# Optimization experiments

Measured on AMD Instinct MI355X. Metric: run time of the kernel, lower is better.

## Reference

```python
import jax, jax.numpy as jnp
import numpy as np
from jax import lax

DIM = 192
HEADS = 6
WS = 8
SHIFT = 4
RED = max(8, DIM // 8)  # 24
HID = 4 * DIM


def _rel_index(ws):
    coords = np.stack(np.meshgrid(np.arange(ws), np.arange(ws), indexing='ij'))  # [2,ws,ws]
    flat = coords.reshape(2, -1)
    rel = (flat[:, :, None] - flat[:, None, :]).transpose(1, 2, 0)  # [T,T,2]
    rel[:, :, 0] += ws - 1
    rel[:, :, 1] += ws - 1
    rel[:, :, 0] *= 2 * ws - 1
    return rel.sum(-1)  # [T,T]


def _build_mask(h, w, ws, shift):
    img = np.zeros((h, w))
    slices = (slice(0, -ws), slice(-ws, -shift), slice(-shift, None))
    cnt = 0
    for hs in slices:
        for wcs in slices:
            img[hs, wcs] = cnt
            cnt += 1
    mw = img.reshape(h // ws, ws, w // ws, ws).transpose(0, 2, 1, 3).reshape(-1, ws * ws)
    diff = mw[:, None, :] - mw[:, :, None]  # [nW,T,T], diff[w,i,j]=mw[w,j]-mw[w,i]
    return np.where(diff != 0, -100.0, 0.0).astype(np.float32)


def _ln(x, g, b):
    m = x.mean(-1, keepdims=True)
    v = ((x - m) ** 2).mean(-1, keepdims=True)
    return (x - m) / jnp.sqrt(v + 1e-5) * g + b


def _conv(x, k, b, pad):
    y = lax.conv_general_dilated(x, k, (1, 1), [(pad, pad), (pad, pad)],
                                 dimension_numbers=('NCHW', 'OIHW', 'NCHW'))
    return y + b[None, :, None, None]


def setup_inputs() -> dict:
    key = jax.random.key(0)
    ks = jax.random.split(key, 16)
    rn = lambda k, s, sc=0.02: jax.random.normal(k, s, dtype=jnp.float32) * sc
    C = DIM
    return {
        'x': jax.random.normal(ks[0], (4, 256 * 256, C), dtype=jnp.float32),
        'ln1_g': jnp.ones((C,), jnp.float32), 'ln1_b': jnp.zeros((C,), jnp.float32),
        'w_qkv': rn(ks[1], (3 * C, C)), 'b_qkv': jnp.zeros((3 * C,), jnp.float32),
        'rel_table': rn(ks[2], ((2 * WS - 1) ** 2, HEADS)),
        'w_proj': rn(ks[3], (C, C)), 'b_proj': jnp.zeros((C,), jnp.float32),
        'ln2_g': jnp.ones((C,), jnp.float32), 'ln2_b': jnp.zeros((C,), jnp.float32),
        'w_fc1': rn(ks[4], (HID, C)), 'b_fc1': jnp.zeros((HID,), jnp.float32),
        'w_fc2': rn(ks[5], (C, HID)), 'b_fc2': jnp.zeros((C,), jnp.float32),
        'conv1_w': rn(ks[6], (RED, C, 1, 1)), 'conv1_b': jnp.zeros((RED,), jnp.float32),
        'conv2_w': rn(ks[7], (RED, RED, 3, 3)), 'conv2_b': jnp.zeros((RED,), jnp.float32),
        'conv3_w': rn(ks[8], (C, RED, 1, 1)), 'conv3_b': jnp.zeros((C,), jnp.float32),
        'se_w1': rn(ks[9], (RED, C)), 'se_w2': rn(ks[10], (C, RED)),
        'h': 256, 'w': 256,
    }


def reference(x, ln1_g, ln1_b, w_qkv, b_qkv, rel_table, w_proj, b_proj,
              ln2_g, ln2_b, w_fc1, b_fc1, w_fc2, b_fc2,
              conv1_w, conv1_b, conv2_w, conv2_b, conv3_w, conv3_b,
              se_w1, se_w2, h, w):
    B, _, C = x.shape
    ws, T, nh = WS, WS * WS, HEADS
    hd = C // nh
    scale = hd ** -0.5

    nx = _ln(x, ln1_g, ln1_b).reshape(B, h, w, C)
    local = nx.transpose(0, 3, 1, 2)  # NCHW for LCE

    # shifted window attention
    sh = jnp.roll(nx, (-SHIFT, -SHIFT), axis=(1, 2))
    win = sh.reshape(B, h // ws, ws, w // ws, ws, C).transpose(0, 1, 3, 2, 4, 5).reshape(-1, T, C)
    qkv = (win @ w_qkv.T + b_qkv).reshape(-1, T, 3, nh, hd).transpose(2, 0, 3, 1, 4)
    q, k, v = qkv[0] * scale, qkv[1], qkv[2]  # [BW, nh, T, hd]
    attn = jnp.einsum('whid,whjd->whij', q, k)  # [BW, nh, T, T]
    bias = rel_table[_rel_index(ws).reshape(-1)].reshape(T, T, nh).transpose(2, 0, 1)
    attn = attn + bias[None]
    mask = jnp.asarray(_build_mask(h, w, ws, SHIFT))  # [nW, T, T]
    nW = mask.shape[0]
    attn = attn.reshape(B, nW, nh, T, T) + mask[None, :, None]
    attn = jax.nn.softmax(attn, axis=-1).reshape(-1, nh, T, T)
    out = jnp.einsum('whij,whjd->whid', attn, v).transpose(0, 2, 1, 3).reshape(-1, T, C)
    out = out @ w_proj.T + b_proj
    out = out.reshape(B, h // ws, w // ws, ws, ws, C).transpose(0, 1, 3, 2, 4, 5).reshape(B, h, w, C)
    out = jnp.roll(out, (SHIFT, SHIFT), axis=(1, 2))

    x1 = x + out.reshape(B, h * w, C)
    n2 = _ln(x1, ln2_g, ln2_b)
    mlp = jax.nn.gelu(n2 @ w_fc1.T + b_fc1, approximate=False) @ w_fc2.T + b_fc2
    x2 = x1 + mlp

    # LocalContextExtractor (SE-style)
    y = _conv(local, conv1_w, conv1_b, 0)
    y = _conv(y, conv2_w, conv2_b, 1)
    y = _conv(y, conv3_w, conv3_b, 0)
    y = jnp.where(y >= 0, y, 0.2 * y)  # LeakyReLU(0.2)
    pooled = y.mean(axis=(2, 3))  # [B, C]
    wgt = jax.nn.sigmoid(jax.nn.relu(pooled @ se_w1.T) @ se_w2.T)
    y = y * wgt[:, :, None, None]
    lc = y.reshape(B, C, h * w).transpose(0, 2, 1)
    return x2 + lc
```

## Files before the change

### kernel.cpp

```cpp
#include <hip/hip_runtime.h>
#include <hip/hip_bf16.h>

typedef unsigned short u16;
typedef unsigned long long u64;
typedef __attribute__((ext_vector_type(8))) short short8x;
typedef __attribute__((ext_vector_type(4))) float f32x4;
typedef __bf16 bf16x8 __attribute__((ext_vector_type(8)));

#define SCALE 0.17677669529663687f

__device__ __forceinline__ u16 f2bf(float f) {
  unsigned u = __builtin_bit_cast(unsigned, f);
  unsigned r = (u + 0x7FFFu + ((u >> 16) & 1u)) >> 16;
  return (u16)r;
}
__device__ __forceinline__ float bf2f(u16 h) {
  return __builtin_bit_cast(float, ((unsigned)h) << 16);
}
__device__ __forceinline__ float gelu_f(float v) {
  float t = v * v;
  float a = __builtin_fmaf(t, -0.07135481627f, -1.59576912161f);
  float e = __expf(v * a);
  return v * __builtin_amdgcn_rcpf(1.0f + e);
}
__device__ __forceinline__ int swz(int row, int col, int ld) {
  return row * ld + ((((col >> 3) ^ (row & 7)) << 3) | (col & 7));
}
__device__ __forceinline__ short8x ldfrag(const u16* s, int row, int kb, int ld) {
  return *(const short8x*)(s + row * ld + (((kb >> 3) ^ (row & 7)) << 3));
}
__device__ __forceinline__ short8x ldg8(const u16* p) { return *(const short8x*)p; }

__device__ __forceinline__ f32x4 MFMA(short8x a, short8x b, f32x4 c) {
  return __builtin_amdgcn_mfma_f32_16x16x32_bf16(
      __builtin_bit_cast(bf16x8, a), __builtin_bit_cast(bf16x8, b), c, 0, 0, 0);
}
__device__ __forceinline__ u64 pack4(float a, float b, float c, float d) {
  return (u64)f2bf(a) | ((u64)f2bf(b) << 16) | ((u64)f2bf(c) << 32) | ((u64)f2bf(d) << 48);
}

__global__ void cvt_kernel(const float* __restrict__ wqkv, const float* __restrict__ wproj,
                           const float* __restrict__ wfc1, const float* __restrict__ wfc2,
                           const float* __restrict__ c1, const float* __restrict__ c3,
                           const float* __restrict__ c2,
                           u16* oq, u16* op, u16* o1, u16* o2, u16* oc1, u16* oc3,
                           float* ow2r) {
  int i = blockIdx.x * 256 + threadIdx.x;
  if (i < 110592) { float f = wqkv[i]; if (i < 36864) f *= SCALE; oq[i] = f2bf(f); return; }
  i -= 110592;
  if (i < 36864) { op[i] = f2bf(wproj[i]); return; }
  i -= 36864;
  if (i < 147456) { o1[i] = f2bf(wfc1[i]); return; }
  i -= 147456;
  if (i < 147456) { o2[i] = f2bf(wfc2[i]); return; }
  i -= 147456;
  if (i < 6144) { int r = i / 192, c = i - r * 192; oc1[i] = (r < 24) ? f2bf(c1[r * 192 + c]) : (u16)0; return; }
  i -= 6144;
  if (i < 6144) { int cc = i >> 5, k = i & 31; oc3[i] = (k < 24) ? f2bf(c3[cc * 24 + k]) : (u16)0; return; }
  i -= 6144;
  if (i < 5184) { int t = i / 576, rr = i - t * 576; int ci = rr / 24, co = rr - ci * 24;
                  ow2r[i] = c2[co * 216 + ci * 9 + t]; }
}

__global__ __launch_bounds__(256) void ln1_kernel(const float* __restrict__ x,
                                                  const float* __restrict__ g,
                                                  const float* __restrict__ b,
                                                  u16* __restrict__ nx) {
  const int wid = threadIdx.x >> 6, lane = threadIdx.x & 63;
  const int row = blockIdx.x * 4 + wid;
  const float* xr = x + row * 192;
  f32x4 v = {0.f, 0.f, 0.f, 0.f};
  if (lane < 48) v = *(const f32x4*)(xr + lane * 4);
  float s = v[0] + v[1] + v[2] + v[3];
  for (int m = 1; m < 64; m <<= 1) s += __shfl_xor(s, m);
  const float mean = s * (1.0f / 192.0f);
  f32x4 d;
#pragma unroll
  for (int r = 0; r < 4; ++r) d[r] = v[r] - mean;
  float q = (lane < 48) ? (d[0] * d[0] + d[1] * d[1] + d[2] * d[2] + d[3] * d[3]) : 0.f;
  for (int m = 1; m < 64; m <<= 1) q += __shfl_xor(q, m);
  const float rstd = rsqrtf(q * (1.0f / 192.0f) + 1e-5f);
  if (lane < 48) {
    const f32x4 gg = *(const f32x4*)(g + lane * 4);
    const f32x4 bb = *(const f32x4*)(b + lane * 4);
    u64 pk = pack4(d[0] * rstd * gg[0] + bb[0], d[1] * rstd * gg[1] + bb[1],
                   d[2] * rstd * gg[2] + bb[2], d[3] * rstd * gg[3] + bb[3]);
    *(u64*)(nx + row * 192 + lane * 4) = pk;
  }
}

__global__ __launch_bounds__(512, 4) void attn_kernel(
    const float* __restrict__ x, const u16* __restrict__ nx,
    const u16* __restrict__ wq, const float* __restrict__ bqkv,
    const float* __restrict__ rel, const u16* __restrict__ wp,
    const float* __restrict__ bproj, u16* __restrict__ vT,
    float* __restrict__ x1out) {
  __shared__ u16 sQK[64 * 384];
  __shared__ u16 sRel[1350];
  __shared__ int sG[64];

  const int tid = threadIdx.x, blk = blockIdx.x;
  const int b = blk >> 10, wi = (blk >> 5) & 31, wj = blk & 31;
  const int wv = tid >> 6, lane = tid & 63, lr = lane & 15, hi = lane >> 4;
  u16* vTw = vT + blk * 12288;

  for (int i = tid; i < 1350; i += 512) sRel[i] = f2bf(rel[i]);
  if (tid < 64) {
    int si = (wi * 8 + (tid >> 3) + 4) & 255, sj = (wj * 8 + (tid & 7) + 4) & 255;
    sG[tid] = b * 65536 + si * 256 + sj;
  }
  for (int i = tid; i < 64 * 96; i += 512) {
    int r = i / 96, w32 = i - r * 96;
    int si = (wi * 8 + (r >> 3) + 4) & 255, sj = (wj * 8 + (r & 7) + 4) & 255;
    int grow = b * 65536 + si * 256 + sj;
    unsigned v = ((const unsigned*)nx)[grow * 96 + w32];
    ((unsigned*)sQK)[r * 192 + ((((w32 >> 2) ^ (r & 7)) << 2) | (w32 & 3))] = v;
  }
  __syncthreads();

  f32x4 acc[4][4] = {};
  if (wv < 6) {
    const int wbase = wv * 64;
#pragma unroll
    for (int kk = 0; kk < 6; ++kk) {
      short8x Xf[4];
#pragma unroll
      for (int tt = 0; tt < 4; ++tt) Xf[tt] = ldfrag(sQK, tt * 16 + lr, kk * 32 + hi * 8, 384);
#pragma unroll
      for (int wt = 0; wt < 4; ++wt) {
        short8x Wf = ldg8(wq + (wbase + wt * 16 + lr) * 192 + kk * 32 + hi * 8);
#pragma unroll
        for (int tt = 0; tt < 4; ++tt) acc[wt][tt] = MFMA(Wf, Xf[tt], acc[wt][tt]);
      }
    }
  } else {
    const int vbase = (wv - 6) * 96;
#pragma unroll
    for (int half = 0; half < 2; ++half) {
      short8x Bf[3][6];
      float bv[3];
#pragma unroll
      for (int j = 0; j < 3; ++j) {
        const int vc = vbase + (half * 3 + j) * 16 + lr;
#pragma unroll
        for (int kk = 0; kk < 6; ++kk)
          Bf[j][kk] = ldg8(wq + (384 + vc) * 192 + kk * 32 + hi * 8);
        bv[j] = bqkv[384 + vc];
      }
#pragma unroll
      for (int mt = 0; mt < 4; ++mt) {
        f32x4 vacc[3] = {};
#pragma unroll
        for (int kk = 0; kk < 6; ++kk) {
          short8x A = ldfrag(sQK, mt * 16 + lr, kk * 32 + hi * 8, 384);
#pragma unroll
          for (int j = 0; j < 3; ++j) vacc[j] = MFMA(A, Bf[j][kk], vacc[j]);
        }
#pragma unroll
        for (int j = 0; j < 3; ++j) {
          u64 pk = pack4(vacc[j][0] + bv[j], vacc[j][1] + bv[j],
                         vacc[j][2] + bv[j], vacc[j][3] + bv[j]);
          *(u64*)(vTw + (vbase + (half * 3 + j) * 16 + lr) * 64 + mt * 16 + hi * 4) = pk;
        }
      }
    }
  }
  __syncthreads();

  if (wv < 6) {
    const int wbase = wv * 64;
#pragma unroll
    for (int wt = 0; wt < 4; ++wt) {
      const int oc0 = wbase + wt * 16 + hi * 4;
      const f32x4 bq = *(const f32x4*)(bqkv + oc0);
      const float sc = (oc0 < 192) ? SCALE : 1.0f;
#pragma unroll
      for (int tt = 0; tt < 4; ++tt) {
        u64 pk = pack4(acc[wt][tt][0] + bq[0] * sc, acc[wt][tt][1] + bq[1] * sc,
                       acc[wt][tt][2] + bq[2] * sc, acc[wt][tt][3] + bq[3] * sc);
        *(u64*)&sQK[swz(tt * 16 + lr, oc0, 384)] = pk;
      }
    }
  }
  __syncthreads();

  f32x4 S[3][4];
#pragma unroll
  for (int i = 0; i < 3; ++i) {
    const int s = wv + 8 * i, h3 = s >> 2, q = s & 3;
    short8x Aq = ldfrag(sQK, q * 16 + lr, h3 * 32 + hi * 8, 384);
#pragma unroll
    for (int nt = 0; nt < 4; ++nt) {
      short8x Bk = ldfrag(sQK, nt * 16 + lr, 192 + h3 * 32 + hi * 8, 384);
      S[i][nt] = MFMA(Aq, Bk, (f32x4){0.f, 0.f, 0.f, 0.f});
    }
#pragma unroll
    for (int r = 0; r < 4; ++r) {
      const int tI = q * 16 + hi * 4 + r;
      const int tri = tI >> 3, trj = tI & 7;
      const int ui = wi * 8 + tri, vi = wj * 8 + trj;
      const int rgi = (ui >= 248) + (ui >= 252), cgi = (vi >= 248) + (vi >= 252);
#pragma unroll
      for (int nt = 0; nt < 4; ++nt) {
        const int tJ = nt * 16 + lr;
        const int tci = tJ >> 3, tcj = tJ & 7;
        const int idx = (tri - tci + 7) * 15 + (trj - tcj + 7);
        float v = S[i][nt][r] + bf2f(sRel[idx * 6 + h3]);
        const int uj = wi * 8 + tci, vj = wj * 8 + tcj;
        const int rgj = (uj >= 248) + (uj >= 252), cgj = (vj >= 248) + (vj >= 252);
        if ((rgi != rgj) | (cgi != cgj)) v -= 100.0f;
        S[i][nt][r] = v;
      }
    }
#pragma unroll
    for (int r = 0; r < 4; ++r) {
      float mx = fmaxf(fmaxf(S[i][0][r], S[i][1][r]), fmaxf(S[i][2][r], S[i][3][r]));
      mx = fmaxf(mx, __shfl_xor(mx, 1));
      mx = fmaxf(mx, __shfl_xor(mx, 2));
      mx = fmaxf(mx, __shfl_xor(mx, 4));
      mx = fmaxf(mx, __shfl_xor(mx, 8));
      float sm = 0.f;
#pragma unroll
      for (int nt = 0; nt < 4; ++nt) { float e = __expf(S[i][nt][r] - mx); S[i][nt][r] = e; sm += e; }
      sm += __shfl_xor(sm, 1); sm += __shfl_xor(sm, 2);
      sm += __shfl_xor(sm, 4); sm += __shfl_xor(sm, 8);
      const float inv = 1.0f / sm;
#pragma unroll
      for (int nt = 0; nt < 4; ++nt) S[i][nt][r] *= inv;
    }
  }
  __syncthreads();

#pragma unroll
  for (int i = 0; i < 3; ++i) {
    const int s = wv + 8 * i, h3 = s >> 2, q = s & 3;
#pragma unroll
    for (int r = 0; r < 4; ++r)
#pragma unroll
      for (int nt = 0; nt < 4; ++nt)
        sQK[h3 * 4096 + swz(q * 16 + hi * 4 + r, nt * 16 + lr, 64)] = f2bf(S[i][nt][r]);
  }
  __syncthreads();

  f32x4 oacc[3][2] = {};
#pragma unroll
  for (int i = 0; i < 3; ++i) {
    const int t = wv + 8 * i, h3 = t >> 2, dt = (t >> 1) & 1, tth = t & 1;
#pragma unroll
    for (int kk = 0; kk < 2; ++kk) {
      short8x Va = ldg8(vTw + (h3 * 32 + dt * 16 + lr) * 64 + kk * 32 + hi * 8);
#pragma unroll
      for (int t2 = 0; t2 < 2; ++t2) {
        short8x Pf = ldfrag(sQK + h3 * 4096, tth * 32 + t2 * 16 + lr, kk * 32 + hi * 8, 64);
        oacc[i][t2] = MFMA(Va, Pf, oacc[i][t2]);
      }
    }
  }
  __syncthreads();

#pragma unroll
  for (int i = 0; i < 3; ++i) {
    const int t = wv + 8 * i, h3 = t >> 2, dt = (t >> 1) & 1, tth = t & 1;
#pragma unroll
    for (int t2 = 0; t2 < 2; ++t2) {
      u64 pk = pack4(oacc[i][t2][0], oacc[i][t2][1], oacc[i][t2][2], oacc[i][t2][3]);
      *(u64*)&sQK[swz(tth * 32 + t2 * 16 + lr, h3 * 32 + dt * 16 + hi * 4, 192)] = pk;
    }
  }
  __syncthreads();

  {
    const int nw = (wv < 4) ? 2 : 1;
    const int wt0 = (wv < 4) ? wv * 2 : (4 + wv);
    f32x4 pacc[2][4] = {};
#pragma unroll
    for (int kk = 0; kk < 6; ++kk) {
      short8x Of[4];
#pragma unroll
      for (int tt = 0; tt < 4; ++tt) Of[tt] = ldfrag(sQK, tt * 16 + lr, kk * 32 + hi * 8, 192);
      for (int w2 = 0; w2 < nw; ++w2) {
        short8x Wp = ldg8(wp + ((wt0 + w2) * 16 + lr) * 192 + kk * 32 + hi * 8);
#pragma unroll
        for (int tt = 0; tt < 4; ++tt) pacc[w2][tt] = MFMA(Wp, Of[tt], pacc[w2][tt]);
      }
    }
    for (int w2 = 0; w2 < nw; ++w2) {
      const int oc0 = (wt0 + w2) * 16 + hi * 4;
      const f32x4 bb = *(const f32x4*)(bproj + oc0);
#pragma unroll
      for (int tt = 0; tt < 4; ++tt) {
        const int grow = sG[tt * 16 + lr];
        const f32x4 xv = *(const f32x4*)(x + grow * 192 + oc0);
        f32x4 o;
#pragma unroll
        for (int r = 0; r < 4; ++r) o[r] = xv[r] + pacc[w2][tt][r] + bb[r];
        *(f32x4*)(x1out + grow * 192 + oc0) = o;
      }
    }
  }
}

__global__ __launch_bounds__(256) void conv1_kernel(const u16* __restrict__ nx,
                                                    const u16* __restrict__ w1,
                                                    const float* __restrict__ b1,
                                                    float* __restrict__ y1) {
  const int tid = threadIdx.x, wv = tid >> 6, lane = tid & 63, lr = lane & 15, hi = lane >> 4;
  const int g0 = blockIdx.x * 64;
  const int mt = wv;
  short8x Af[6];
#pragma unroll
  for (int kk = 0; kk < 6; ++kk)
    Af[kk] = ldg8(nx + (g0 + mt * 16 + lr) * 192 + kk * 32 + hi * 8);
  const int bI = g0 >> 16;
  const int hw0 = g0 & 65535;
#pragma unroll
  for (int nt = 0; nt < 2; ++nt) {
    f32x4 acc = {0.f, 0.f, 0.f, 0.f};
#pragma unroll
    for (int kk = 0; kk < 6; ++kk) {
      short8x Bf = ldg8(w1 + (nt * 16 + lr) * 192 + kk * 32 + hi * 8);
      acc = MFMA(Af[kk], Bf, acc);
    }
    const int c = nt * 16 + lr;
    if (c < 24) {
      const float bb = b1[c];
#pragma unroll
      for (int r = 0; r < 4; ++r) {
        const int pix = hw0 + mt * 16 + hi * 4 + r;
        y1[(bI * 24 + c) * 65536 + pix] = acc[r] + bb;
      }
    }
  }
}

__global__ __launch_bounds__(256) void conv2_kernel(const float* __restrict__ y1,
                                                    const float* __restrict__ w2r,
                                                    const float* __restrict__ cb2,
                                                    u16* __restrict__ y2) {
  const int j = threadIdx.x;
  const int i = blockIdx.x & 255;
  const int b = blockIdx.x >> 8;
  float acc[24];
#pragma unroll
  for (int r = 0; r < 24; ++r) acc[r] = cb2[r];
  const float* base = y1 + b * 24 * 65536;
  for (int t = 0; t < 9; ++t) {
    const int dh = t / 3 - 1, dw = t % 3 - 1;
    const int ii = i + dh, jj = j + dw;
    const bool ok = (ii >= 0) & (ii < 256) & (jj >= 0) & (jj < 256);
    const int offc = ok ? (ii * 256 + jj) : 0;
    const float* wt = w2r + t * 576;
    float v[24];
#pragma unroll
    for (int ci = 0; ci < 24; ++ci) {
      float vv = base[ci * 65536 + offc];
      v[ci] = ok ? vv : 0.0f;
    }
#pragma unroll
    for (int ci = 0; ci < 24; ++ci)
#pragma unroll
      for (int co = 0; co < 24; ++co)
        acc[co] += v[ci] * wt[ci * 24 + co];
  }
  u16* o = y2 + (b * 65536 + i * 256 + j) * 32;
#pragma unroll
  for (int r = 0; r < 24; ++r) o[r] = f2bf(acc[r]);
  ((unsigned long long*)(o + 24))[0] = 0ull;
  ((unsigned long long*)(o + 24))[1] = 0ull;
}

__global__ __launch_bounds__(256) void conv3_kernel(const u16* __restrict__ y2,
                                                    const u16* __restrict__ w3,
                                                    const float* __restrict__ b3,
                                                    u16* __restrict__ y,
                                                    float* __restrict__ pooled) {
  const int tid = threadIdx.x, wv = tid >> 6, lane = tid & 63, lr = lane & 15, hi = lane >> 4;
  const int g0 = blockIdx.x * 64;
  short8x Af[4];
#pragma unroll
  for (int mt = 0; mt < 4; ++mt)
    Af[mt] = ldg8(y2 + (g0 + mt * 16 + lr) * 32 + hi * 8);
  const int bI = g0 >> 16;
#pragma unroll
  for (int nt0 = 0; nt0 < 3; ++nt0) {
    const int c = (wv * 3 + nt0) * 16 + lr;
    short8x Bf = ldg8(w3 + c * 32 + hi * 8);
    const float bb = b3[c];
    float colsum = 0.f;
#pragma unroll
    for (int mt = 0; mt < 4; ++mt) {
      f32x4 acc = {0.f, 0.f, 0.f, 0.f};
      acc = MFMA(Af[mt], Bf, acc);
#pragma unroll
      for (int r = 0; r < 4; ++r) {
        float v = acc[r] + bb;
        v = (v >= 0.f) ? v : 0.2f * v;
        y[(g0 + mt * 16 + hi * 4 + r) * 192 + c] = f2bf(v);
        colsum += v;
      }
    }
    colsum += __shfl_xor(colsum, 16);
    colsum += __shfl_xor(colsum, 32);
    if (hi == 0) atomicAdd(&pooled[bI * 192 + c], colsum);
  }
}

__global__ void se_kernel(const float* __restrict__ pooled, const float* __restrict__ w1,
                          const float* __restrict__ w2, float* __restrict__ wgt) {
  __shared__ float t[24];
  const int b = blockIdx.x, lane = threadIdx.x;
  if (lane < 24) {
    float s = 0.f;
    for (int c = 0; c < 192; ++c) s += pooled[b * 192 + c] * (1.0f / 65536.0f) * w1[lane * 192 + c];
    t[lane] = fmaxf(s, 0.0f);
  }
  __syncthreads();
  for (int c = lane; c < 192; c += 64) {
    float s = 0.f;
#pragma unroll
    for (int r = 0; r < 24; ++r) s += t[r] * w2[c * 24 + r];
    wgt[b * 192 + c] = 1.0f / (1.0f + __expf(-s));
  }
}

__global__ __launch_bounds__(768, 6) void mlp_kernel(
    const float* x1, const float* __restrict__ g2, const float* __restrict__ b2,
    const u16* __restrict__ w1m, const float* __restrict__ bf1,
    const u16* __restrict__ w2m, const float* __restrict__ bf2,
    const u16* __restrict__ y, const float* __restrict__ wgt, float* out) {
  __shared__ u16 sN[64 * 192];
  __shared__ u16 sH[64 * 192];
  const int tid = threadIdx.x, wv = tid >> 6, lane = tid & 63, lr = lane & 15, hi = lane >> 4;
  const int g0 = blockIdx.x * 64;

  for (int row = wv; row < 64; row += 12) {
    const float* xr = x1 + (g0 + row) * 192;
    f32x4 v = {0.f, 0.f, 0.f, 0.f};
    if (lane < 48) v = *(const f32x4*)(xr + lane * 4);
    float s = v[0] + v[1] + v[2] + v[3];
    for (int m = 1; m < 64; m <<= 1) s += __shfl_xor(s, m);
    const float mean = s * (1.0f / 192.0f);
    f32x4 d;
#pragma unroll
    for (int r = 0; r < 4; ++r) d[r] = v[r] - mean;
    float q = (lane < 48) ? (d[0] * d[0] + d[1] * d[1] + d[2] * d[2] + d[3] * d[3]) : 0.f;
    for (int m = 1; m < 64; m <<= 1) q += __shfl_xor(q, m);
    const float rstd = rsqrtf(q * (1.0f / 192.0f) + 1e-5f);
    if (lane < 48) {
      const f32x4 gg = *(const f32x4*)(g2 + lane * 4);
      const f32x4 bb = *(const f32x4*)(b2 + lane * 4);
      u64 pk = pack4(d[0] * rstd * gg[0] + bb[0], d[1] * rstd * gg[1] + bb[1],
                     d[2] * rstd * gg[2] + bb[2], d[3] * rstd * gg[3] + bb[3]);
      *(u64*)&sN[swz(row, lane * 4, 192)] = pk;
    }
  }
  __syncthreads();

  f32x4 acc[4] = {};
  for (int c = 0; c < 4; ++c) {
    const int hcol = c * 192 + wv * 16 + lr;
    f32x4 a1[4] = {};
#pragma unroll
    for (int kk = 0; kk < 6; ++kk) {
      short8x B = ldg8(w1m + hcol * 192 + kk * 32 + hi * 8);
#pragma unroll
      for (int mt = 0; mt < 4; ++mt)
        a1[mt] = MFMA(ldfrag(sN, mt * 16 + lr, kk * 32 + hi * 8, 192), B, a1[mt]);
    }
    if (c) __syncthreads();
    const float bb1 = bf1[hcol];
#pragma unroll
    for (int mt = 0; mt < 4; ++mt)
#pragma unroll
      for (int r = 0; r < 4; ++r)
        sH[swz(mt * 16 + hi * 4 + r, wv * 16 + lr, 192)] = f2bf(gelu_f(a1[mt][r] + bb1));
    __syncthreads();
#pragma unroll
    for (int kk = 0; kk < 6; ++kk) {
      short8x B = ldg8(w2m + (wv * 16 + lr) * 768 + c * 192 + kk * 32 + hi * 8);
#pragma unroll
      for (int mt = 0; mt < 4; ++mt)
        acc[mt] = MFMA(ldfrag(sH, mt * 16 + lr, kk * 32 + hi * 8, 192), B, acc[mt]);
    }
  }

  const int bI = g0 >> 16;
  const int ocol = wv * 16 + lr;
  const float bb = bf2[ocol];
  const float wg = wgt[bI * 192 + ocol];
#pragma unroll
  for (int mt = 0; mt < 4; ++mt)
#pragma unroll
    for (int r = 0; r < 4; ++r) {
      const int grow = g0 + mt * 16 + hi * 4 + r;
      const float lc = bf2f(y[grow * 192 + ocol]) * wg;
      out[grow * 192 + ocol] = x1[grow * 192 + ocol] + acc[mt][r] + bb + lc;
    }
}

extern "C" void kernel_launch(void* const* d_in, const int* in_sizes, int n_in,
                              void* d_out, int out_size, void* d_ws, size_t ws_size,
                              hipStream_t stream) {
  const float* x     = (const float*)d_in[0];
  const float* ln1g  = (const float*)d_in[1];
  const float* ln1b  = (const float*)d_in[2];
  const float* wqkv  = (const float*)d_in[3];
  const float* bqkv  = (const float*)d_in[4];
  const float* rel   = (const float*)d_in[5];
  const float* wproj = (const float*)d_in[6];
  const float* bproj = (const float*)d_in[7];
  const float* ln2g  = (const float*)d_in[8];
  const float* ln2b  = (const float*)d_in[9];
  const float* wfc1  = (const float*)d_in[10];
  const float* bfc1  = (const float*)d_in[11];
  const float* wfc2  = (const float*)d_in[12];
  const float* bfc2  = (const float*)d_in[13];
  const float* c1w   = (const float*)d_in[14];
  const float* c1b   = (const float*)d_in[15];
  const float* c2w   = (const float*)d_in[16];
  const float* c2b   = (const float*)d_in[17];
  const float* c3w   = (const float*)d_in[18];
  const float* c3b   = (const float*)d_in[19];
  const float* sew1  = (const float*)d_in[20];
  const float* sew2  = (const float*)d_in[21];

  char* ws = (char*)d_ws;
  u16*   nx   = (u16*)(ws + 0);
  float* y1   = (float*)(ws + 100663296);
  u16*   y2   = (u16*)(ws + 125829120);
  u16*   yb   = (u16*)(ws + 142606336);
  u16*   wq   = (u16*)(ws + 243269632);
  u16*   wp   = (u16*)(ws + 243490816);
  u16*   w1m  = (u16*)(ws + 243564544);
  u16*   w2m  = (u16*)(ws + 243859456);
  u16*   cw1  = (u16*)(ws + 244154368);
  u16*   cw3  = (u16*)(ws + 244166656);
  float* w2r  = (float*)(ws + 244178944);
  float* pool = (float*)(ws + 244199680);
  float* wgt  = (float*)(ws + 244202752);
  float* out  = (float*)d_out;
  u16*   vT   = yb;

  hipMemsetAsync(pool, 0, 3072, stream);
  cvt_kernel<<<1797, 256, 0, stream>>>(wqkv, wproj, wfc1, wfc2, c1w, c3w, c2w,
                                       wq, wp, w1m, w2m, cw1, cw3, w2r);
  ln1_kernel<<<65536, 256, 0, stream>>>(x, ln1g, ln1b, nx);
  attn_kernel<<<4096, 512, 0, stream>>>(x, nx, wq, bqkv, rel, wp, bproj, vT, out);
  conv1_kernel<<<4096, 256, 0, stream>>>(nx, cw1, c1b, y1);
  conv2_kernel<<<1024, 256, 0, stream>>>(y1, w2r, c2b, y2);
  conv3_kernel<<<4096, 256, 0, stream>>>(y2, cw3, c3b, yb, pool);
  se_kernel<<<4, 64, 0, stream>>>(pool, sew1, sew2, wgt);
  mlp_kernel<<<4096, 768, 0, stream>>>(out, ln2g, ln2b, w1m, bfc1, w2m, bfc2, yb, wgt, out);
}
```

Baseline: 1.031 ms.

## Fuse LayerNorm1 with conv1 and move 3x3 conv2 onto bf16 MFMA

LayerNorm1 and the 1x1 conv1 now run in one kernel: normalized rows are kept in swizzled shared memory and fed straight to the MFMA conv, so nx is no longer re-read from global memory. The scalar fp32 3x3 conv2 becomes an MFMA implicit GEMM. Each block stages a 3-row by 66-column halo tile of y1 as bf16 in LDS, and the weights are repacked into padded bf16 32x32 matrices per tap. This removes redundant global reads and slow scalar FMAs, at the cost of bf16 rounding of the conv2 inputs and weights.

```diff
diff --git a/kernel.cpp b/kernel.cpp
--- a/kernel.cpp
+++ b/kernel.cpp
@@ -44,7 +44,7 @@
                            const float* __restrict__ c1, const float* __restrict__ c3,
                            const float* __restrict__ c2,
                            u16* oq, u16* op, u16* o1, u16* o2, u16* oc1, u16* oc3,
-                           float* ow2r) {
+                           u16* ow2b) {
   int i = blockIdx.x * 256 + threadIdx.x;
   if (i < 110592) { float f = wqkv[i]; if (i < 36864) f *= SCALE; oq[i] = f2bf(f); return; }
   i -= 110592;
@@ -58,34 +58,67 @@
   i -= 6144;
   if (i < 6144) { int cc = i >> 5, k = i & 31; oc3[i] = (k < 24) ? f2bf(c3[cc * 24 + k]) : (u16)0; return; }
   i -= 6144;
-  if (i < 5184) { int t = i / 576, rr = i - t * 576; int ci = rr / 24, co = rr - ci * 24;
-                  ow2r[i] = c2[co * 216 + ci * 9 + t]; }
-}
-
-__global__ __launch_bounds__(256) void ln1_kernel(const float* __restrict__ x,
-                                                  const float* __restrict__ g,
-                                                  const float* __restrict__ b,
-                                                  u16* __restrict__ nx) {
-  const int wid = threadIdx.x >> 6, lane = threadIdx.x & 63;
-  const int row = blockIdx.x * 4 + wid;
-  const float* xr = x + row * 192;
-  f32x4 v = {0.f, 0.f, 0.f, 0.f};
-  if (lane < 48) v = *(const f32x4*)(xr + lane * 4);
-  float s = v[0] + v[1] + v[2] + v[3];
-  for (int m = 1; m < 64; m <<= 1) s += __shfl_xor(s, m);
-  const float mean = s * (1.0f / 192.0f);
-  f32x4 d;
-#pragma unroll
-  for (int r = 0; r < 4; ++r) d[r] = v[r] - mean;
-  float q = (lane < 48) ? (d[0] * d[0] + d[1] * d[1] + d[2] * d[2] + d[3] * d[3]) : 0.f;
-  for (int m = 1; m < 64; m <<= 1) q += __shfl_xor(q, m);
-  const float rstd = rsqrtf(q * (1.0f / 192.0f) + 1e-5f);
-  if (lane < 48) {
-    const f32x4 gg = *(const f32x4*)(g + lane * 4);
-    const f32x4 bb = *(const f32x4*)(b + lane * 4);
-    u64 pk = pack4(d[0] * rstd * gg[0] + bb[0], d[1] * rstd * gg[1] + bb[1],
-                   d[2] * rstd * gg[2] + bb[2], d[3] * rstd * gg[3] + bb[3]);
-    *(u64*)(nx + row * 192 + lane * 4) = pk;
+  if (i < 9216) {
+    int t = i >> 10, rr = i & 1023, co = rr >> 5, ci = rr & 31;
+    ow2b[i] = (co < 24 && ci < 24) ? f2bf(c2[co * 216 + ci * 9 + t]) : (u16)0;
+  }
+}
+
+__global__ __launch_bounds__(256) void lnc1_kernel(
+    const float* __restrict__ x, const float* __restrict__ g,
+    const float* __restrict__ b, const u16* __restrict__ w1,
+    const float* __restrict__ cb1, u16* __restrict__ nx, float* __restrict__ y1) {
+  __shared__ u16 sN[64 * 192];
+  const int tid = threadIdx.x, wv = tid >> 6, lane = tid & 63, lr = lane & 15, hi = lane >> 4;
+  const int g0 = blockIdx.x * 64;
+
+  for (int row = wv; row < 64; row += 4) {
+    const float* xr = x + (g0 + row) * 192;
+    f32x4 v = {0.f, 0.f, 0.f, 0.f};
+    if (lane < 48) v = *(const f32x4*)(xr + lane * 4);
+    float s = v[0] + v[1] + v[2] + v[3];
+    for (int m = 1; m < 64; m <<= 1) s += __shfl_xor(s, m);
+    const float mean = s * (1.0f / 192.0f);
+    f32x4 d;
+#pragma unroll
+    for (int r = 0; r < 4; ++r) d[r] = v[r] - mean;
+    float q = (lane < 48) ? (d[0] * d[0] + d[1] * d[1] + d[2] * d[2] + d[3] * d[3]) : 0.f;
+    for (int m = 1; m < 64; m <<= 1) q += __shfl_xor(q, m);
+    const float rstd = rsqrtf(q * (1.0f / 192.0f) + 1e-5f);
+    if (lane < 48) {
+      const f32x4 gg = *(const f32x4*)(g + lane * 4);
+      const f32x4 bb = *(const f32x4*)(b + lane * 4);
+      u64 pk = pack4(d[0] * rstd * gg[0] + bb[0], d[1] * rstd * gg[1] + bb[1],
+                     d[2] * rstd * gg[2] + bb[2], d[3] * rstd * gg[3] + bb[3]);
+      *(u64*)(nx + (g0 + row) * 192 + lane * 4) = pk;
+      *(u64*)&sN[swz(row, lane * 4, 192)] = pk;
+    }
+  }
+  __syncthreads();
+
+  short8x Af[6];
+#pragma unroll
+  for (int kk = 0; kk < 6; ++kk)
+    Af[kk] = ldfrag(sN, wv * 16 + lr, kk * 32 + hi * 8, 192);
+  const int bI = g0 >> 16;
+  const int hw0 = g0 & 65535;
+#pragma unroll
+  for (int nt = 0; nt < 2; ++nt) {
+    f32x4 acc = {0.f, 0.f, 0.f, 0.f};
+#pragma unroll
+    for (int kk = 0; kk < 6; ++kk) {
+      short8x Bf = ldg8(w1 + (nt * 16 + lr) * 192 + kk * 32 + hi * 8);
+      acc = MFMA(Af[kk], Bf, acc);
+    }
+    const int c = nt * 16 + lr;
+    if (c < 24) {
+      const float bb = cb1[c];
+#pragma unroll
+      for (int r = 0; r < 4; ++r) {
+        const int pix = hw0 + wv * 16 + hi * 4 + r;
+        y1[(bI * 24 + c) * 65536 + pix] = acc[r] + bb;
+      }
+    }
   }
 }
 
@@ -300,73 +333,48 @@
   }
 }
 
-__global__ __launch_bounds__(256) void conv1_kernel(const u16* __restrict__ nx,
-                                                    const u16* __restrict__ w1,
-                                                    const float* __restrict__ b1,
-                                                    float* __restrict__ y1) {
-  const int tid = threadIdx.x, wv = tid >> 6, lane = tid & 63, lr = lane & 15, hi = lane >> 4;
-  const int g0 = blockIdx.x * 64;
-  const int mt = wv;
-  short8x Af[6];
-#pragma unroll
-  for (int kk = 0; kk < 6; ++kk)
-    Af[kk] = ldg8(nx + (g0 + mt * 16 + lr) * 192 + kk * 32 + hi * 8);
-  const int bI = g0 >> 16;
-  const int hw0 = g0 & 65535;
-#pragma unroll
-  for (int nt = 0; nt < 2; ++nt) {
-    f32x4 acc = {0.f, 0.f, 0.f, 0.f};
-#pragma unroll
-    for (int kk = 0; kk < 6; ++kk) {
-      short8x Bf = ldg8(w1 + (nt * 16 + lr) * 192 + kk * 32 + hi * 8);
-      acc = MFMA(Af[kk], Bf, acc);
-    }
-    const int c = nt * 16 + lr;
-    if (c < 24) {
-      const float bb = b1[c];
-#pragma unroll
-      for (int r = 0; r < 4; ++r) {
-        const int pix = hw0 + mt * 16 + hi * 4 + r;
-        y1[(bI * 24 + c) * 65536 + pix] = acc[r] + bb;
-      }
-    }
-  }
-}
-
 __global__ __launch_bounds__(256) void conv2_kernel(const float* __restrict__ y1,
-                                                    const float* __restrict__ w2r,
+                                                    const u16* __restrict__ w2b,
                                                     const float* __restrict__ cb2,
                                                     u16* __restrict__ y2) {
-  const int j = threadIdx.x;
-  const int i = blockIdx.x & 255;
-  const int b = blockIdx.x >> 8;
-  float acc[24];
-#pragma unroll
-  for (int r = 0; r < 24; ++r) acc[r] = cb2[r];
-  const float* base = y1 + b * 24 * 65536;
+  __shared__ u16 sA[3 * 66 * 32];
+  const int tid = threadIdx.x, wv = tid >> 6, lane = tid & 63, lr = lane & 15, hi = lane >> 4;
+  const int blk = blockIdx.x;
+  const int b = blk >> 10, rem = blk & 1023, i = rem >> 2, j0 = (rem & 3) << 6;
+
+  for (int t = tid; t < 6336; t += 256) {
+    const int ci = t / 198, rest = t - ci * 198, ro = rest / 66, p = rest - ro * 66;
+    const int ii = i + ro - 1, jj = j0 - 1 + p;
+    float val = 0.f;
+    if (ci < 24 && ii >= 0 && ii < 256 && jj >= 0 && jj < 256)
+      val = y1[((b * 24 + ci) << 16) + ii * 256 + jj];
+    sA[ro * 2112 + p * 32 + ((((ci >> 3) ^ (p & 3)) << 3) | (ci & 7))] = f2bf(val);
+  }
+  __syncthreads();
+
+  f32x4 acc[2] = {};
+#pragma unroll
   for (int t = 0; t < 9; ++t) {
-    const int dh = t / 3 - 1, dw = t % 3 - 1;
-    const int ii = i + dh, jj = j + dw;
-    const bool ok = (ii >= 0) & (ii < 256) & (jj >= 0) & (jj < 256);
-    const int offc = ok ? (ii * 256 + jj) : 0;
-    const float* wt = w2r + t * 576;
-    float v[24];
-#pragma unroll
-    for (int ci = 0; ci < 24; ++ci) {
-      float vv = base[ci * 65536 + offc];
-      v[ci] = ok ? vv : 0.0f;
-    }
-#pragma unroll
-    for (int ci = 0; ci < 24; ++ci)
-#pragma unroll
-      for (int co = 0; co < 24; ++co)
-        acc[co] += v[ci] * wt[ci * 24 + co];
-  }
-  u16* o = y2 + (b * 65536 + i * 256 + j) * 32;
-#pragma unroll
-  for (int r = 0; r < 24; ++r) o[r] = f2bf(acc[r]);
-  ((unsigned long long*)(o + 24))[0] = 0ull;
-  ((unsigned long long*)(o + 24))[1] = 0ull;
+    const int dh = t / 3, dw = t % 3;
+    const int pl = wv * 16 + lr + dw;
+    short8x Af = *(const short8x*)(sA + dh * 2112 + pl * 32 + ((hi ^ (pl & 3)) << 3));
+#pragma unroll
+    for (int nt = 0; nt < 2; ++nt) {
+      short8x Bf = ldg8(w2b + t * 1024 + (nt * 16 + lr) * 32 + hi * 8);
+      acc[nt] = MFMA(Af, Bf, acc[nt]);
+    }
+  }
+  const int pixbase = b * 65536 + i * 256 + j0 + wv * 16 + hi * 4;
+#pragma unroll
+  for (int nt = 0; nt < 2; ++nt) {
+    const int c = nt * 16 + lr;
+    const float bb = (c < 24) ? cb2[c] : 0.f;
+#pragma unroll
+    for (int r = 0; r < 4; ++r) {
+      float val = (c < 24) ? (acc[nt][r] + bb) : 0.f;
+      y2[(pixbase + r) * 32 + c] = f2bf(val);
+    }
+  }
 }
 
 __global__ __launch_bounds__(256) void conv3_kernel(const u16* __restrict__ y2,
@@ -535,19 +543,18 @@
   u16*   w2m  = (u16*)(ws + 243859456);
   u16*   cw1  = (u16*)(ws + 244154368);
   u16*   cw3  = (u16*)(ws + 244166656);
-  float* w2r  = (float*)(ws + 244178944);
+  u16*   w2b  = (u16*)(ws + 244178944);
   float* pool = (float*)(ws + 244199680);
   float* wgt  = (float*)(ws + 244202752);
   float* out  = (float*)d_out;
   u16*   vT   = yb;
 
   hipMemsetAsync(pool, 0, 3072, stream);
-  cvt_kernel<<<1797, 256, 0, stream>>>(wqkv, wproj, wfc1, wfc2, c1w, c3w, c2w,
-                                       wq, wp, w1m, w2m, cw1, cw3, w2r);
-  ln1_kernel<<<65536, 256, 0, stream>>>(x, ln1g, ln1b, nx);
+  cvt_kernel<<<1812, 256, 0, stream>>>(wqkv, wproj, wfc1, wfc2, c1w, c3w, c2w,
+                                       wq, wp, w1m, w2m, cw1, cw3, w2b);
+  lnc1_kernel<<<4096, 256, 0, stream>>>(x, ln1g, ln1b, cw1, c1b, nx, y1);
   attn_kernel<<<4096, 512, 0, stream>>>(x, nx, wq, bqkv, rel, wp, bproj, vT, out);
-  conv1_kernel<<<4096, 256, 0, stream>>>(nx, cw1, c1b, y1);
-  conv2_kernel<<<1024, 256, 0, stream>>>(y1, w2r, c2b, y2);
+  conv2_kernel<<<4096, 256, 0, stream>>>(y1, w2b, c2b, y2);
   conv3_kernel<<<4096, 256, 0, stream>>>(y2, cw3, c3b, yb, pool);
   se_kernel<<<4, 64, 0, stream>>>(pool, sew1, sew2, wgt);
   mlp_kernel<<<4096, 768, 0, stream>>>(out, ln2g, ln2b, w1m, bfc1, w2m, bfc2, yb, wgt, out);
```

After: 1.017 ms. No clear change (-1.4%).
